# Kernel optimization log

Measured on AMD Instinct MI355X. Metric: run time of the kernel, lower is better.

The kernel has to match this reference:

```python
import jax, jax.numpy as jnp
import numpy as np

T, D, DFF = 8192, 512, 2048
EPS = 1e-5
LS_INIT = 1e-4

def setup_inputs() -> dict:
    key = jax.random.key(0)
    ks = jax.random.split(key, 5)
    s = 0.02
    return {
        "x": jax.random.normal(ks[0], (T, D), jnp.float32),
        "W_in": jax.random.normal(ks[1], (3 * D, D), jnp.float32) * s,
        "W_out": jax.random.normal(ks[2], (D, D), jnp.float32) * s,
        "W1": jax.random.normal(ks[3], (DFF, D), jnp.float32) * s,
        "W2": jax.random.normal(ks[4], (D, DFF), jnp.float32) * s,
        "g1": jnp.ones((D,), jnp.float32),
        "b1": jnp.zeros((D,), jnp.float32),
        "g2": jnp.ones((D,), jnp.float32),
        "b2": jnp.zeros((D,), jnp.float32),
        "ls1": jnp.full((D,), LS_INIT, jnp.float32),
        "ls2": jnp.full((D,), LS_INIT, jnp.float32),
    }

def _layer_norm(x, g, b):
    mu = jnp.mean(x, axis=-1, keepdims=True)
    var = jnp.mean((x - mu) ** 2, axis=-1, keepdims=True)
    return (x - mu) * jax.lax.rsqrt(var + EPS) * g + b

def reference(x, W_in, W_out, W1, W2, g1, b1, g2, b2, ls1, ls2):
    t = x.shape[0]
    # --- self-attention block (faithful: no head split, no 1/sqrt(d) scale, k @ q^T) ---
    h = _layer_norm(x, g1, b1)                       # [T, D]
    proj = h @ W_in.T                                # [T, 3D]
    q, k, v = jnp.split(proj, 3, axis=-1)            # each [T, D]
    scores = k @ q.T                                 # [T, T]
    mask = jnp.tril(jnp.ones((t, t), scores.dtype))
    scores = jnp.where(mask == 0, -jnp.inf, scores)
    attn = jax.nn.softmax(scores, axis=-1)
    o = (attn @ v) @ W_out.T                         # [T, D]
    x = x + ls1 * o
    # --- FFN block ---
    h = _layer_norm(x, g2, b2)
    update = jax.nn.gelu(h @ W1.T) @ W2.T            # [T, D]
    return x + ls2 * update
```

## Files before the change

kernel.cpp:

```cpp
#include <hip/hip_runtime.h>
#include <hip/hip_bf16.h>


using bf16 = __hip_bfloat16;
typedef __attribute__((ext_vector_type(8))) short short8;
typedef __attribute__((ext_vector_type(4))) float f32x4;

#define T_DIM 8192

#define AS1C(p) (const __attribute__((address_space(1))) void*)(p)
#define AS3P(p) (__attribute__((address_space(3))) void*)(p)
#define GLL16(src, dst) __builtin_amdgcn_global_load_lds(AS1C(src), AS3P(dst), 16, 0, 0)

static __device__ __forceinline__ short f2bfbits(float f) {
  bf16 b = __float2bfloat16(f);
  short s; __builtin_memcpy(&s, &b, 2); return s;
}
static __device__ __forceinline__ float bfbits2f(short s) {
  unsigned u = ((unsigned)(unsigned short)s) << 16;
  float f; __builtin_memcpy(&f, &u, 4); return f;
}

__global__ void cvt4_kernel(
    const float* __restrict__ a, bf16* __restrict__ oa, int na,
    const float* __restrict__ b, bf16* __restrict__ ob, int nb,
    const float* __restrict__ c, bf16* __restrict__ oc, int nc,
    const float* __restrict__ d, bf16* __restrict__ od, int nd)
{
  int i = blockIdx.x * 256 + threadIdx.x;
  if (i < na) { oa[i] = __float2bfloat16(a[i]); return; }
  i -= na;
  if (i < nb) { ob[i] = __float2bfloat16(b[i]); return; }
  i -= nb;
  if (i < nc) { oc[i] = __float2bfloat16(c[i]); return; }
  i -= nc;
  if (i < nd) od[i] = __float2bfloat16(d[i]);
}

__global__ __launch_bounds__(256) void ln_kernel(
    const float* __restrict__ x, const float* __restrict__ g,
    const float* __restrict__ bb, bf16* __restrict__ h)
{
  const int row = blockIdx.x * 4 + (threadIdx.x >> 6);
  const int lane = threadIdx.x & 63;
  const float* xr = x + (size_t)row * 512 + lane * 8;
  f32x4 v0 = *(const f32x4*)xr;
  f32x4 v1 = *(const f32x4*)(xr + 4);
  float s = 0.f;
#pragma unroll
  for (int j = 0; j < 4; ++j) s += v0[j] + v1[j];
#pragma unroll
  for (int d = 1; d < 64; d <<= 1) s += __shfl_xor(s, d);
  const float mu = s * (1.f / 512.f);
  float vs = 0.f;
#pragma unroll
  for (int j = 0; j < 4; ++j) { float a = v0[j] - mu, b2 = v1[j] - mu; vs += a * a + b2 * b2; }
#pragma unroll
  for (int d = 1; d < 64; d <<= 1) vs += __shfl_xor(vs, d);
  const float rs = rsqrtf(vs * (1.f / 512.f) + 1e-5f);
  const f32x4 g0 = *(const f32x4*)(g + lane * 8);
  const f32x4 g1v = *(const f32x4*)(g + lane * 8 + 4);
  const f32x4 b0 = *(const f32x4*)(bb + lane * 8);
  const f32x4 b1v = *(const f32x4*)(bb + lane * 8 + 4);
  short8 ov;
#pragma unroll
  for (int j = 0; j < 4; ++j) {
    ov[j]     = f2bfbits((v0[j] - mu) * rs * g0[j] + b0[j]);
    ov[j + 4] = f2bfbits((v1[j] - mu) * rs * g1v[j] + b1v[j]);
  }
  *(short8*)(h + (size_t)row * 512 + lane * 8) = ov;
}

enum { MODE_BF16 = 0, MODE_GELU = 1, MODE_RESID = 2 };

static __device__ __forceinline__ float gelu_f(float x) {
  float x3 = x * x * x;
  float t = tanhf(0.7978845608028654f * (x + 0.044715f * x3));
  return 0.5f * x * (1.0f + t);
}

template <int MODE>
__global__ __launch_bounds__(256, 2) void gemm_bt(
    const bf16* __restrict__ A, const bf16* __restrict__ B,
    int M, int N, int K,
    bf16* __restrict__ Cb, float* __restrict__ Cf,
    const float* __restrict__ resid, const float* __restrict__ scale)
{
  __shared__ bf16 sA[128 * 64];
  __shared__ bf16 sB[128 * 64];
  const int tid = threadIdx.x;
  const int lane = tid & 63, wave = tid >> 6;
  const int bm = blockIdx.x, bn = blockIdx.y;
  const int wm = (wave & 1) * 64, wn = (wave >> 1) * 64;
  const int ln = lane & 15, lg = lane >> 4;
  f32x4 acc[4][4] = {};

  const int nkt = K >> 6;
  for (int kt = 0; kt < nkt; ++kt) {
    __syncthreads();
#pragma unroll
    for (int r = 0; r < 4; ++r) {
      const int s = r * 256 + tid;
      const int ks = s >> 9, rb = (s >> 6) & 7, l = s & 63;
      const bf16* srcA = A + (size_t)(bm * 128 + rb * 16 + (l & 15)) * K + kt * 64 + ks * 32 + (l >> 4) * 8;
      GLL16(srcA, sA + (size_t)(r * 256 + wave * 64) * 8);
      const bf16* srcB = B + (size_t)(bn * 128 + rb * 16 + (l & 15)) * K + kt * 64 + ks * 32 + (l >> 4) * 8;
      GLL16(srcB, sB + (size_t)(r * 256 + wave * 64) * 8);
    }
    __syncthreads();
#pragma unroll
    for (int ks = 0; ks < 2; ++ks) {
      short8 af[4], bfr[4];
#pragma unroll
      for (int mi = 0; mi < 4; ++mi)
        af[mi] = *(const short8*)(sA + (size_t)(ks * 512 + ((wm >> 4) + mi) * 64 + lane) * 8);
#pragma unroll
      for (int ni = 0; ni < 4; ++ni)
        bfr[ni] = *(const short8*)(sB + (size_t)(ks * 512 + ((wn >> 4) + ni) * 64 + lane) * 8);
#pragma unroll
      for (int mi = 0; mi < 4; ++mi)
#pragma unroll
        for (int ni = 0; ni < 4; ++ni)
          acc[mi][ni] = __builtin_amdgcn_mfma_f32_16x16x32_bf16(af[mi], bfr[ni], acc[mi][ni], 0, 0, 0);
    }
  }
#pragma unroll
  for (int mi = 0; mi < 4; ++mi) {
#pragma unroll
    for (int ni = 0; ni < 4; ++ni) {
#pragma unroll
      for (int r = 0; r < 4; ++r) {
        const int row = bm * 128 + wm + mi * 16 + lg * 4 + r;
        const int col = bn * 128 + wn + ni * 16 + ln;
        const size_t idx = (size_t)row * N + col;
        float v = acc[mi][ni][r];
        if constexpr (MODE == MODE_GELU) { Cb[idx] = __float2bfloat16(gelu_f(v)); }
        else if constexpr (MODE == MODE_RESID) { Cf[idx] = resid[idx] + scale[col] * v; }
        else { Cb[idx] = __float2bfloat16(v); }
      }
    }
  }
}

__global__ __launch_bounds__(256) void transpose_v(const bf16* __restrict__ proj, bf16* __restrict__ vT) {
  __shared__ bf16 tile[64][66];
  const int t0 = blockIdx.x * 64, d0 = blockIdx.y * 64;
  const int tid = threadIdx.x;
#pragma unroll
  for (int i = 0; i < 16; ++i) {
    const int lin = i * 256 + tid;
    const int r = lin >> 6, c = lin & 63;
    tile[r][c] = proj[(size_t)(t0 + r) * 1536 + 1024 + d0 + c];
  }
  __syncthreads();
#pragma unroll
  for (int i = 0; i < 16; ++i) {
    const int lin = i * 256 + tid;
    const int dy = lin >> 6, tx = lin & 63;
    vT[(size_t)(d0 + dy) * T_DIM + t0 + tx] = tile[tx][dy];
  }
}

__global__ __launch_bounds__(512, 2) void attn_kernel(
    const bf16* __restrict__ proj, const bf16* __restrict__ vT,
    bf16* __restrict__ Op, float* __restrict__ mlp)
{
  __shared__ bf16 sQ[2][32 * 512];
  __shared__ bf16 sV[2][32 * 512];
  __shared__ bf16 sP[8][16 * 40];

  const int tid = threadIdx.x, lane = tid & 63, wave = tid >> 6;
  const int ln = lane & 15, lg = lane >> 4;
  const int b = 511 - blockIdx.x;
  const int it = b >> 3;
  const int ch = b & 7;
  const int nj = 4 * it + 4;
  const int jlo = ch * nj / 8;
  const int jhi = (ch + 1) * nj / 8;
  const int wrow = it * 128 + wave * 16;

  short8 kf[16];
#pragma unroll
  for (int ks = 0; ks < 16; ++ks)
    kf[ks] = *(const short8*)(proj + (size_t)(wrow + ln) * 1536 + 512 + ks * 32 + lg * 8);

  f32x4 oa[32] = {};
  float m_r[4] = {-__builtin_inff(), -__builtin_inff(), -__builtin_inff(), -__builtin_inff()};
  float l_r[4] = {0.f, 0.f, 0.f, 0.f};

  auto stageQ = [&](int c, int jt) {
    const int j0 = jt * 32;
#pragma unroll
    for (int r = 0; r < 4; ++r) {
      const int s = r * 512 + tid;
      const int l = s & 63;
      const int ks = s >> 7, jb = (s >> 6) & 1;
      const bf16* srcQ = proj + (size_t)(j0 + jb * 16 + (l & 15)) * 1536 + ks * 32 + (l >> 4) * 8;
      GLL16(srcQ, &sQ[c][(size_t)(r * 512 + wave * 64) * 8]);
    }
  };
  auto stageV = [&](int c, int jt) {
    const int j0 = jt * 32;
#pragma unroll
    for (int r = 0; r < 4; ++r) {
      const int s = r * 512 + tid;
      const int l = s & 63;
      const int nb = s >> 6;
      const bf16* srcV = vT + (size_t)(nb * 16 + (l & 15)) * T_DIM + j0 + (l >> 4) * 8;
      GLL16(srcV, &sV[c][(size_t)(r * 512 + wave * 64) * 8]);
    }
  };

  if (jlo < jhi) {
    int cur = 0;
    stageQ(0, jlo);
    stageV(0, jlo);
    for (int jt = jlo; jt < jhi; ++jt) {
      const int j0 = jt * 32;
      const bool more = (jt + 1 < jhi);
      if (more) stageQ(cur ^ 1, jt + 1);
      if (more) { asm volatile("s_waitcnt vmcnt(8)" ::: "memory"); }
      else      { asm volatile("s_waitcnt vmcnt(4)" ::: "memory"); }
      __builtin_amdgcn_s_barrier();
      __builtin_amdgcn_sched_barrier(0);
      if (j0 <= wrow + 15) {
        f32x4 sfr[2] = {};
        __builtin_amdgcn_s_setprio(1);
#pragma unroll
        for (int ks = 0; ks < 16; ++ks) {
          short8 q0 = *(const short8*)(&sQ[cur][(size_t)(ks * 128 + lane) * 8]);
          short8 q1 = *(const short8*)(&sQ[cur][(size_t)(ks * 128 + 64 + lane) * 8]);
          sfr[0] = __builtin_amdgcn_mfma_f32_16x16x32_bf16(kf[ks], q0, sfr[0], 0, 0, 0);
          sfr[1] = __builtin_amdgcn_mfma_f32_16x16x32_bf16(kf[ks], q1, sfr[1], 0, 0, 0);
        }
        __builtin_amdgcn_s_setprio(0);
        if (j0 + 31 > wrow) {
#pragma unroll
          for (int jb = 0; jb < 2; ++jb)
#pragma unroll
            for (int r = 0; r < 4; ++r) {
              const int i = wrow + lg * 4 + r, j = j0 + jb * 16 + ln;
              if (j > i) sfr[jb][r] = -__builtin_inff();
            }
        }
        float mx[4], sc[4], mm[4];
#pragma unroll
        for (int r = 0; r < 4; ++r) mx[r] = fmaxf(sfr[0][r], sfr[1][r]);
#pragma unroll
        for (int d = 1; d < 16; d <<= 1)
#pragma unroll
          for (int r = 0; r < 4; ++r) mx[r] = fmaxf(mx[r], __shfl_xor(mx[r], d));
#pragma unroll
        for (int r = 0; r < 4; ++r) {
          mm[r] = fmaxf(fmaxf(m_r[r], mx[r]), -1e30f);
          sc[r] = __expf(m_r[r] - mm[r]);
          m_r[r] = mm[r];
          l_r[r] *= sc[r];
        }
        float ts[4] = {0.f, 0.f, 0.f, 0.f};
#pragma unroll
        for (int jb = 0; jb < 2; ++jb)
#pragma unroll
          for (int r = 0; r < 4; ++r) {
            float p = __expf(sfr[jb][r] - mm[r]);
            sfr[jb][r] = p;
            ts[r] += p;
          }
#pragma unroll
        for (int d = 1; d < 16; d <<= 1)
#pragma unroll
          for (int r = 0; r < 4; ++r) ts[r] += __shfl_xor(ts[r], d);
#pragma unroll
        for (int r = 0; r < 4; ++r) l_r[r] += ts[r];
#pragma unroll
        for (int jb = 0; jb < 2; ++jb)
#pragma unroll
          for (int r = 0; r < 4; ++r)
            sP[wave][(lg * 4 + r) * 40 + jb * 16 + ln] = __float2bfloat16(sfr[jb][r]);
#pragma unroll
        for (int nb = 0; nb < 32; ++nb)
#pragma unroll
          for (int r = 0; r < 4; ++r) oa[nb][r] *= sc[r];
      }
      if (more) stageV(cur ^ 1, jt + 1);
      if (more) { asm volatile("s_waitcnt vmcnt(8)" ::: "memory"); }
      else      { asm volatile("s_waitcnt vmcnt(0)" ::: "memory"); }
      __builtin_amdgcn_s_barrier();
      __builtin_amdgcn_sched_barrier(0);
      if (j0 <= wrow + 15) {
        const short8 pa = *(const short8*)(&sP[wave][0] + ln * 40 + lg * 8);
        __builtin_amdgcn_s_setprio(1);
#define LDV(nb) (*(const short8*)(&sV[cur][(size_t)((nb) * 64 + lane) * 8]))
        short8 vf0 = LDV(0), vf1 = LDV(1), vf2 = LDV(2), vf3 = LDV(3);
#pragma unroll
        for (int nb = 0; nb < 28; nb += 4) {
          const short8 w0 = vf0, w1 = vf1, w2 = vf2, w3 = vf3;
          vf0 = LDV(nb + 4); vf1 = LDV(nb + 5); vf2 = LDV(nb + 6); vf3 = LDV(nb + 7);
          oa[nb]     = __builtin_amdgcn_mfma_f32_16x16x32_bf16(pa, w0, oa[nb],     0, 0, 0);
          oa[nb + 1] = __builtin_amdgcn_mfma_f32_16x16x32_bf16(pa, w1, oa[nb + 1], 0, 0, 0);
          oa[nb + 2] = __builtin_amdgcn_mfma_f32_16x16x32_bf16(pa, w2, oa[nb + 2], 0, 0, 0);
          oa[nb + 3] = __builtin_amdgcn_mfma_f32_16x16x32_bf16(pa, w3, oa[nb + 3], 0, 0, 0);
        }
        oa[28] = __builtin_amdgcn_mfma_f32_16x16x32_bf16(pa, vf0, oa[28], 0, 0, 0);
        oa[29] = __builtin_amdgcn_mfma_f32_16x16x32_bf16(pa, vf1, oa[29], 0, 0, 0);
        oa[30] = __builtin_amdgcn_mfma_f32_16x16x32_bf16(pa, vf2, oa[30], 0, 0, 0);
        oa[31] = __builtin_amdgcn_mfma_f32_16x16x32_bf16(pa, vf3, oa[31], 0, 0, 0);
#undef LDV
        __builtin_amdgcn_s_setprio(0);
      }
      cur ^= 1;
    }
  }
#pragma unroll
  for (int nb = 0; nb < 32; ++nb)
#pragma unroll
    for (int r = 0; r < 4; ++r)
      Op[((size_t)ch * T_DIM + wrow + lg * 4 + r) * 512 + nb * 16 + ln] = __float2bfloat16(oa[nb][r]);
  if (ln == 0) {
#pragma unroll
    for (int r = 0; r < 4; ++r) {
      mlp[((size_t)ch * T_DIM + wrow + lg * 4 + r) * 2 + 0] = m_r[r];
      mlp[((size_t)ch * T_DIM + wrow + lg * 4 + r) * 2 + 1] = l_r[r];
    }
  }
}

__global__ __launch_bounds__(256) void combine_kernel(
    const bf16* __restrict__ Op, const float* __restrict__ mlp, bf16* __restrict__ o)
{
  const int row = blockIdx.x * 4 + (threadIdx.x >> 6);
  const int lane = threadIdx.x & 63;
  const int k = 8;
  float m = -__builtin_inff();
  for (int c = 0; c < k; ++c) m = fmaxf(m, mlp[((size_t)c * T_DIM + row) * 2]);
  float l = 0.f;
  for (int c = 0; c < k; ++c) {
    const float mc = mlp[((size_t)c * T_DIM + row) * 2];
    const float lc = mlp[((size_t)c * T_DIM + row) * 2 + 1];
    l += __expf(mc - m) * lc;
  }
  const float inv = 1.0f / l;
  f32x4 a0 = {}, a1 = {};
  for (int c = 0; c < k; ++c) {
    const float w = __expf(mlp[((size_t)c * T_DIM + row) * 2] - m);
    const short8 u = *(const short8*)(Op + ((size_t)c * T_DIM + row) * 512 + lane * 8);
#pragma unroll
    for (int j = 0; j < 4; ++j) {
      a0[j] += w * bfbits2f(u[j]);
      a1[j] += w * bfbits2f(u[j + 4]);
    }
  }
  short8 ov;
#pragma unroll
  for (int j = 0; j < 4; ++j) {
    ov[j]     = f2bfbits(a0[j] * inv);
    ov[j + 4] = f2bfbits(a1[j] * inv);
  }
  *(short8*)(o + (size_t)row * 512 + lane * 8) = ov;
}

extern "C" void kernel_launch(void* const* d_in, const int* in_sizes, int n_in,
                              void* d_out, int out_size, void* d_ws, size_t ws_size,
                              hipStream_t stream) {
  (void)in_sizes; (void)n_in; (void)out_size; (void)ws_size;
  const float* x    = (const float*)d_in[0];
  const float* Win  = (const float*)d_in[1];
  const float* Wout = (const float*)d_in[2];
  const float* W1   = (const float*)d_in[3];
  const float* W2   = (const float*)d_in[4];
  const float* g1   = (const float*)d_in[5];
  const float* b1   = (const float*)d_in[6];
  const float* g2   = (const float*)d_in[7];
  const float* b2   = (const float*)d_in[8];
  const float* ls1  = (const float*)d_in[9];
  const float* ls2  = (const float*)d_in[10];
  float* out = (float*)d_out;

  char* w = (char*)d_ws;
  size_t off = 0;
  auto alloc = [&](size_t bytes) -> char* {
    char* p = w + off; off += (bytes + 255) & ~(size_t)255; return p;
  };
  bf16* wWin  = (bf16*)alloc((size_t)1536 * 512 * 2);
  bf16* wWout = (bf16*)alloc((size_t)512 * 512 * 2);
  bf16* wW1   = (bf16*)alloc((size_t)2048 * 512 * 2);
  bf16* wW2   = (bf16*)alloc((size_t)512 * 2048 * 2);
  bf16* h     = (bf16*)alloc((size_t)T_DIM * 512 * 2);
  bf16* proj  = (bf16*)alloc((size_t)T_DIM * 1536 * 2);
  bf16* vTb   = (bf16*)alloc((size_t)512 * T_DIM * 2);
  bf16* o     = (bf16*)alloc((size_t)T_DIM * 512 * 2);
  float* x1   = (float*)alloc((size_t)T_DIM * 512 * 4);
  bf16* Op    = (bf16*)alloc((size_t)8 * T_DIM * 512 * 2);
  float* mlp  = (float*)alloc((size_t)8 * T_DIM * 2 * 4);
  bf16* f1 = proj;

  cvt4_kernel<<<(1536 * 512 + 512 * 512 + 2048 * 512 + 512 * 2048 + 255) / 256, 256, 0, stream>>>(
      Win, wWin, 1536 * 512, Wout, wWout, 512 * 512,
      W1, wW1, 2048 * 512, W2, wW2, 512 * 2048);

  ln_kernel<<<T_DIM / 4, 256, 0, stream>>>(x, g1, b1, h);
  gemm_bt<MODE_BF16><<<dim3(64, 12), 256, 0, stream>>>(h, wWin, 8192, 1536, 512, proj, nullptr, nullptr, nullptr);
  transpose_v<<<dim3(T_DIM / 64, 8), 256, 0, stream>>>(proj, vTb);
  attn_kernel<<<512, 512, 0, stream>>>(proj, vTb, Op, mlp);
  combine_kernel<<<T_DIM / 4, 256, 0, stream>>>(Op, mlp, o);
  gemm_bt<MODE_RESID><<<dim3(64, 4), 256, 0, stream>>>(o, wWout, 8192, 512, 512, nullptr, x1, x, ls1);
  ln_kernel<<<T_DIM / 4, 256, 0, stream>>>(x1, g2, b2, h);
  gemm_bt<MODE_GELU><<<dim3(64, 16), 256, 0, stream>>>(h, wW1, 8192, 2048, 512, f1, nullptr, nullptr, nullptr);
  gemm_bt<MODE_RESID><<<dim3(64, 4), 256, 0, stream>>>(f1, wW2, 8192, 512, 2048, nullptr, out, x1, ls2);
}
```

Before: 329.1 us.

## Vectorize weight conversion, swizzle GEMM tiles, skip softmax rescale unless max grows

Three unrelated changes. The fp32-to-bf16 weight conversion now handles four elements per thread with vector loads and stores. The GEMM maps workgroup IDs through a swizzle across eight groups, so that tiles sharing inputs tend to run together and reuse cache. In attention, the online-softmax rescale of the output accumulators is skipped unless some row's new max exceeds the running max by more than 8. That threshold keeps the unnormalized exponentials bounded, and it removes a 128-element multiply per tile in the common case at the cost of a wave-wide branch.

```diff
diff --git a/kernel.cpp b/kernel.cpp
--- a/kernel.cpp
+++ b/kernel.cpp
@@ -4,6 +4,7 @@
 
 using bf16 = __hip_bfloat16;
 typedef __attribute__((ext_vector_type(8))) short short8;
+typedef __attribute__((ext_vector_type(4))) short short4v;
 typedef __attribute__((ext_vector_type(4))) float f32x4;
 
 #define T_DIM 8192
@@ -28,13 +29,20 @@
     const float* __restrict__ d, bf16* __restrict__ od, int nd)
 {
   int i = blockIdx.x * 256 + threadIdx.x;
-  if (i < na) { oa[i] = __float2bfloat16(a[i]); return; }
-  i -= na;
-  if (i < nb) { ob[i] = __float2bfloat16(b[i]); return; }
-  i -= nb;
-  if (i < nc) { oc[i] = __float2bfloat16(c[i]); return; }
-  i -= nc;
-  if (i < nd) od[i] = __float2bfloat16(d[i]);
+  const float* src; bf16* dst;
+  if (i < na / 4) { src = a; dst = oa; }
+  else { i -= na / 4;
+    if (i < nb / 4) { src = b; dst = ob; }
+    else { i -= nb / 4;
+      if (i < nc / 4) { src = c; dst = oc; }
+      else { i -= nc / 4;
+        if (i >= nd / 4) return;
+        src = d; dst = od; } } }
+  const f32x4 v = ((const f32x4*)src)[i];
+  short4v o;
+#pragma unroll
+  for (int j = 0; j < 4; ++j) o[j] = f2bfbits(v[j]);
+  ((short4v*)dst)[i] = o;
 }
 
 __global__ __launch_bounds__(256) void ln_kernel(
@@ -90,7 +98,12 @@
   __shared__ bf16 sB[128 * 64];
   const int tid = threadIdx.x;
   const int lane = tid & 63, wave = tid >> 6;
-  const int bm = blockIdx.x, bn = blockIdx.y;
+  const int NB = gridDim.y;
+  const int nwg = gridDim.x * NB;
+  const int lin = blockIdx.y * gridDim.x + blockIdx.x;
+  const int q8 = nwg >> 3;
+  const int swz = (lin & 7) * q8 + (lin >> 3);
+  const int bm = swz / NB, bn = swz % NB;
   const int wm = (wave & 1) * 64, wn = (wave >> 1) * 64;
   const int ln = lane & 15, lg = lane >> 4;
   f32x4 acc[4][4] = {};
@@ -243,26 +256,36 @@
               if (j > i) sfr[jb][r] = -__builtin_inff();
             }
         }
-        float mx[4], sc[4], mm[4];
+        float mx[4];
 #pragma unroll
         for (int r = 0; r < 4; ++r) mx[r] = fmaxf(sfr[0][r], sfr[1][r]);
 #pragma unroll
         for (int d = 1; d < 16; d <<= 1)
 #pragma unroll
           for (int r = 0; r < 4; ++r) mx[r] = fmaxf(mx[r], __shfl_xor(mx[r], d));
-#pragma unroll
-        for (int r = 0; r < 4; ++r) {
-          mm[r] = fmaxf(fmaxf(m_r[r], mx[r]), -1e30f);
-          sc[r] = __expf(m_r[r] - mm[r]);
-          m_r[r] = mm[r];
-          l_r[r] *= sc[r];
+        bool need = false;
+#pragma unroll
+        for (int r = 0; r < 4; ++r) need |= !(mx[r] - m_r[r] <= 8.0f);
+        if (__any(need)) {
+          float sc[4];
+#pragma unroll
+          for (int r = 0; r < 4; ++r) {
+            float mm = fmaxf(fmaxf(m_r[r], mx[r]), -1e30f);
+            sc[r] = __expf(m_r[r] - mm);
+            m_r[r] = mm;
+            l_r[r] *= sc[r];
+          }
+#pragma unroll
+          for (int nb = 0; nb < 32; ++nb)
+#pragma unroll
+            for (int r = 0; r < 4; ++r) oa[nb][r] *= sc[r];
         }
         float ts[4] = {0.f, 0.f, 0.f, 0.f};
 #pragma unroll
         for (int jb = 0; jb < 2; ++jb)
 #pragma unroll
           for (int r = 0; r < 4; ++r) {
-            float p = __expf(sfr[jb][r] - mm[r]);
+            float p = __expf(sfr[jb][r] - m_r[r]);
             sfr[jb][r] = p;
             ts[r] += p;
           }
@@ -277,10 +300,6 @@
 #pragma unroll
           for (int r = 0; r < 4; ++r)
             sP[wave][(lg * 4 + r) * 40 + jb * 16 + ln] = __float2bfloat16(sfr[jb][r]);
-#pragma unroll
-        for (int nb = 0; nb < 32; ++nb)
-#pragma unroll
-          for (int r = 0; r < 4; ++r) oa[nb][r] *= sc[r];
       }
       if (more) stageV(cur ^ 1, jt + 1);
       if (more) { asm volatile("s_waitcnt vmcnt(8)" ::: "memory"); }
@@ -394,7 +413,7 @@
   float* mlp  = (float*)alloc((size_t)8 * T_DIM * 2 * 4);
   bf16* f1 = proj;
 
-  cvt4_kernel<<<(1536 * 512 + 512 * 512 + 2048 * 512 + 512 * 2048 + 255) / 256, 256, 0, stream>>>(
+  cvt4_kernel<<<(1536 * 512 + 512 * 512 + 2048 * 512 + 512 * 2048) / 4 / 256, 256, 0, stream>>>(
       Win, wWin, 1536 * 512, Wout, wWout, 512 * 512,
       W1, wW1, 2048 * 512, W2, wW2, 512 * 2048);
 
```

Result: faster. 320.3 us (-2.7%).
